# Kernel tuning notes

Measured on AMD Instinct MI355X. Metric: run time of the kernel, lower is better.

Reference implementation:

```python
import jax, jax.numpy as jnp
import numpy as np

B, N, D = 4, 4096, 512          # batch, seq_len, hidden_size
H, DH = 8, 64                    # n_heads, head_dim
M = 512                          # nb_features = 0.125 * seq_len
LN_EPS = 1e-12
KERNEL_EPS = 1e-4


def setup_inputs() -> dict:
    key = jax.random.key(0)
    ks = jax.random.split(key, 12)
    s = 0.02
    return {
        "input_tensor": jax.random.normal(ks[0], (B, N, D), jnp.float32),
        "attention_mask": jnp.zeros((B, 1, 1, N), jnp.float32),  # unused by module
        "Wq": jax.random.normal(ks[1], (D, D), jnp.float32) * s,
        "bq": jnp.zeros((D,), jnp.float32),
        "Wk": jax.random.normal(ks[2], (D, D), jnp.float32) * s,
        "bk": jnp.zeros((D,), jnp.float32),
        "Wv": jax.random.normal(ks[3], (D, D), jnp.float32) * s,
        "bv": jnp.zeros((D,), jnp.float32),
        # gaussian (orthogonal-style) random feature projections [M, DH]
        "proj_q": jax.random.normal(ks[4], (M, DH), jnp.float32),
        "proj_k": jax.random.normal(ks[5], (M, DH), jnp.float32),
        "Wd": jax.random.normal(ks[6], (D, D), jnp.float32) * s,
        "bd": jnp.zeros((D,), jnp.float32),
        "gamma": jnp.ones((D,), jnp.float32),
        "beta": jnp.zeros((D,), jnp.float32),
    }


def _softmax_kernel(data, projection_matrix, is_query):
    # data: [B,H,N,DH], projection_matrix: [M,DH]
    data_normalizer = data.shape[-1] ** (-0.25)
    ratio = projection_matrix.shape[0] ** (-0.5)
    data_dash = jnp.einsum("bhnd,md->bhnm", data_normalizer * data, projection_matrix)
    diag_data = (jnp.sum(data * data, axis=-1) * 0.5 * data_normalizer ** 2)[..., None]
    if is_query:
        stab = jnp.max(data_dash, axis=-1, keepdims=True)
    else:
        stab = jnp.max(data_dash)  # global max, per original code
    return ratio * (jnp.exp(data_dash - diag_data - stab) + KERNEL_EPS)


def _linear_attention(q, k, v):
    # q,k: [B,H,N,M]; v: [B,H,N,DH]
    k_cumsum = jnp.sum(k, axis=-2)                               # [B,H,M]
    d_inv = 1.0 / jnp.einsum("bhnm,bhm->bhn", q, k_cumsum)       # [B,H,N]
    context = jnp.einsum("bhnm,bhne->bhme", k, v)                # [B,H,M,DH]
    return jnp.einsum("bhme,bhnm,bhn->bhne", context, q, d_inv)  # [B,H,N,DH]


def reference(input_tensor, attention_mask, Wq, bq, Wk, bk, Wv, bv,
              proj_q, proj_k, Wd, bd, gamma, beta):
    def heads(x):  # [B,N,D] -> [B,H,N,DH]
        return x.reshape(B, N, H, DH).transpose(0, 2, 1, 3)

    q = heads(input_tensor @ Wq.T + bq)
    k = heads(input_tensor @ Wk.T + bk)
    v = heads(input_tensor @ Wv.T + bv)

    q = _softmax_kernel(q, proj_q, is_query=True)
    k = _softmax_kernel(k, proj_k, is_query=False)

    ctx = _linear_attention(q, k, v)                  # [B,H,N,DH]
    ctx = ctx.transpose(0, 2, 1, 3).reshape(B, N, D)  # merge heads

    hidden = ctx @ Wd.T + bd                          # dropout is identity (eval)
    x = hidden + input_tensor
    mu = jnp.mean(x, axis=-1, keepdims=True)
    var = jnp.mean((x - mu) ** 2, axis=-1, keepdims=True)
    return (x - mu) / jnp.sqrt(var + LN_EPS) * gamma + beta
```

## Files before the change

kernel.cpp:

```cpp
#include <hip/hip_runtime.h>
#include <math.h>

typedef __bf16 bf16;
typedef __bf16 bf16x8 __attribute__((ext_vector_type(8)));
typedef __bf16 bf16x4 __attribute__((ext_vector_type(4)));
typedef float  f32x4  __attribute__((ext_vector_type(4)));

#define NSEQ 4096
#define DMODEL 512
#define DHEAD 64
#define MFEAT 512
#define BHEADS 32
#define ROWS_TOTAL 16384

#define NORMALIZER 0.35355339059327373f
#define DIAG_C 0.0625f
#define KEPS 1e-4f

__device__ __forceinline__ float warpReduceSum(float v) {
#pragma unroll
    for (int off = 32; off > 0; off >>= 1) v += __shfl_xor(v, off);
    return v;
}

__device__ __forceinline__ void atomicMaxF(float* addr, float val) {
    int* ai = (int*)addr;
    int cur = __float_as_int(*addr);
    while (__int_as_float(cur) < val) {
        int prev = atomicCAS(ai, cur, __float_as_int(val));
        if (prev == cur) break;
        cur = prev;
    }
}

__device__ __forceinline__ void gload16(const void* g, void* l) {
    __builtin_amdgcn_global_load_lds((const __attribute__((address_space(1))) void*)g,
                                     (__attribute__((address_space(3))) void*)l, 16, 0, 0);
}

__global__ __launch_bounds__(256)
void prep_convert(const float* __restrict__ x, const float* __restrict__ Wq,
                  const float* __restrict__ Wk, const float* __restrict__ Wv,
                  const float* __restrict__ Wd, const float* __restrict__ pq,
                  const float* __restrict__ bq, const float* __restrict__ bk,
                  const float* __restrict__ bv,
                  bf16* __restrict__ xb, bf16* __restrict__ Wb,
                  bf16* __restrict__ Wdb, bf16* __restrict__ pqb,
                  float* __restrict__ bcat)
{
    size_t i4 = (size_t)blockIdx.x * 256 + threadIdx.x;
    size_t e0 = i4 * 4;
    if (e0 >= 9471488) return;
    const float* src;
    if (e0 < 8388608) {
        src = x + e0;
        float4 v = *(const float4*)src;
        bf16* d = xb + e0;
        d[0] = (bf16)v.x; d[1] = (bf16)v.y; d[2] = (bf16)v.z; d[3] = (bf16)v.w;
    } else if (e0 < 9175040) {
        size_t c = e0 - 8388608; int wsel = (int)(c >> 18); size_t o = c & 262143;
        src = (wsel == 0 ? Wq : wsel == 1 ? Wk : Wv) + o;
        float4 v = *(const float4*)src;
        bf16* d = Wb + c;
        d[0] = (bf16)v.x; d[1] = (bf16)v.y; d[2] = (bf16)v.z; d[3] = (bf16)v.w;
    } else if (e0 < 9437184) {
        size_t c = e0 - 9175040;
        src = Wd + c;
        float4 v = *(const float4*)src;
        bf16* d = Wdb + c;
        d[0] = (bf16)v.x; d[1] = (bf16)v.y; d[2] = (bf16)v.z; d[3] = (bf16)v.w;
    } else if (e0 < 9469952) {
        size_t c = e0 - 9437184;
        src = pq + c;
        float4 v = *(const float4*)src;
        const int feat = (int)(c >> 6), col = (int)(c & 63);
        bf16x4 d4;
        d4[0] = (bf16)v.x; d4[1] = (bf16)v.y; d4[2] = (bf16)v.z; d4[3] = (bf16)v.w;
        const int inrow = (col << 1) ^ ((feat & 7) << 4);
        *(bf16x4*)((char*)pqb + (size_t)feat * 128 + inrow) = d4;
    } else {
        size_t c = e0 - 9469952; int wsel = (int)(c >> 9); size_t o = c & 511;
        src = (wsel == 0 ? bq : wsel == 1 ? bk : bv) + o;
        *(float4*)(bcat + c) = *(const float4*)src;
    }
}

template<int MODE>
__global__ __launch_bounds__(256)
void gemm_mfma(const bf16* __restrict__ A, const bf16* __restrict__ Bw,
               const float* __restrict__ bias, const float* __restrict__ resid,
               bf16* __restrict__ outQ, bf16* __restrict__ outK,
               bf16* __restrict__ outV, float* __restrict__ outF)
{
    __shared__ char As[16384];
    __shared__ char Bs[16384];
    const int tid = threadIdx.x;
    const int w = tid >> 6, l = tid & 63;
    const int wr = w >> 1, wc = w & 1;
    const int row0 = blockIdx.y << 7;
    const int col0 = blockIdx.x << 7;

    f32x4 acc[4][4] = {};
    const char* Ab = (const char*)A + (size_t)row0 * 1024;
    const char* Bb = (const char*)Bw + (size_t)col0 * 1024;

    for (int kt = 0; kt < 8; ++kt) {
        const int k0b = kt << 7;
#pragma unroll
        for (int i = 0; i < 4; ++i) {
            int off = (i << 12) + (tid << 4);
            int g = off ^ ((off >> 3) & 0x70);
            int grow = g >> 7, gcol = g & 127;
            gload16(Ab + (size_t)grow * 1024 + k0b + gcol, As + (i << 12) + (w << 10));
            gload16(Bb + (size_t)grow * 1024 + k0b + gcol, Bs + (i << 12) + (w << 10));
        }
        __syncthreads();
#pragma unroll
        for (int ks = 0; ks < 2; ++ks) {
            bf16x8 af[4], bb[4];
#pragma unroll
            for (int mi = 0; mi < 4; ++mi) {
                int row = (wr << 6) + (mi << 4) + (l & 15);
                int addr = ((row << 7) + (ks << 6) + ((l >> 4) << 4)) ^ ((row & 7) << 4);
                af[mi] = *(const bf16x8*)(As + addr);
            }
#pragma unroll
            for (int nj = 0; nj < 4; ++nj) {
                int row = (wc << 6) + (nj << 4) + (l & 15);
                int addr = ((row << 7) + (ks << 6) + ((l >> 4) << 4)) ^ ((row & 7) << 4);
                bb[nj] = *(const bf16x8*)(Bs + addr);
            }
#pragma unroll
            for (int mi = 0; mi < 4; ++mi)
#pragma unroll
                for (int nj = 0; nj < 4; ++nj)
                    acc[mi][nj] = __builtin_amdgcn_mfma_f32_16x16x32_bf16(af[mi], bb[nj], acc[mi][nj], 0, 0, 0);
        }
        __syncthreads();
    }

    const int subrow = (l >> 4) << 2;
    const int subcol = l & 15;
#pragma unroll
    for (int mi = 0; mi < 4; ++mi) {
#pragma unroll
        for (int nj = 0; nj < 4; ++nj) {
            const int cg = col0 + (wc << 6) + (nj << 4) + subcol;
            const float bi = bias[cg];
            const int rgb = row0 + (wr << 6) + (mi << 4) + subrow;
            if (MODE == 0) {
                if (cg < 512) {
                    const int hh = cg >> 6, ee = cg & 63;
                    const int bb2 = rgb >> 12, n = rgb & 4095;
#pragma unroll
                    for (int r = 0; r < 4; ++r)
                        outQ[((size_t)((bb2 * 8 + hh) * 4096 + n + r)) * 64 + ee] =
                            (bf16)(acc[mi][nj][r] + bi);
                } else if (cg < 1024) {
                    const int eg = cg - 512, hh = eg >> 6, ee = eg & 63;
#pragma unroll
                    for (int r = 0; r < 4; ++r) {
                        const int rg = rgb + r;
                        *(bf16*)((char*)outK + (size_t)rg * 1024 + hh * 128 +
                                 ((ee * 2) ^ ((rg & 7) << 4))) = (bf16)(acc[mi][nj][r] + bi);
                    }
                } else {
                    const int eg = cg - 1024, hh = eg >> 6, ee = eg & 63;
                    const int bb2 = rgb >> 12, n = rgb & 4095;
                    bf16x4 pv;
#pragma unroll
                    for (int r = 0; r < 4; ++r) pv[r] = (bf16)(acc[mi][nj][r] + bi);
                    const int nb = n * 2;
                    size_t byteaddr = (size_t)((bb2 * 8 + hh) * 64 + ee) * 8192
                                    + (size_t)((nb & ~127) | ((nb & 127) ^ ((ee & 7) << 4)));
                    *(bf16x4*)((char*)outV + byteaddr) = pv;
                }
            } else {
#pragma unroll
                for (int r = 0; r < 4; ++r) {
                    const int rg = rgb + r;
                    outF[(size_t)rg * 512 + cg] = acc[mi][nj][r] + bi + resid[(size_t)rg * 512 + cg];
                }
            }
        }
    }
}

__global__ __launch_bounds__(64)
void vsum_kernel(const bf16* __restrict__ Vt, float* __restrict__ vsum)
{
    const int row = blockIdx.x;
    const bf16x8* p = (const bf16x8*)((const char*)Vt + (size_t)row * 8192);
    float s = 0.f;
#pragma unroll
    for (int i = 0; i < 8; ++i) {
        bf16x8 v = p[threadIdx.x + i * 64];
#pragma unroll
        for (int u = 0; u < 8; ++u) s += (float)v[u];
    }
    s = warpReduceSum(s);
    if (threadIdx.x == 0) vsum[row] = s;
}

__global__ __launch_bounds__(256)
void diag_kernel(const bf16* __restrict__ Kb, float* __restrict__ dgk)
{
    const int idx = blockIdx.x * 256 + threadIdx.x;
    const int bh = idx >> 12, n = idx & 4095;
    const int b = bh >> 3, h = bh & 7;
    const char* row = (const char*)Kb + (size_t)(b * 4096 + n) * 1024 + h * 128;
    const int sw = (n & 7) << 4;
    float ss = 0.f;
#pragma unroll
    for (int j = 0; j < 8; ++j) {
        bf16x8 v = *(const bf16x8*)(row + ((j << 4) ^ sw));
#pragma unroll
        for (int u = 0; u < 8; ++u) { float f = (float)v[u]; ss += f * f; }
    }
    dgk[idx] = DIAG_C * ss;
}

__global__ __launch_bounds__(512, 1)
void kside_mfma6(const bf16* __restrict__ Kb, const bf16* __restrict__ Vt,
                 const float* __restrict__ projk, const float* __restrict__ dgk,
                 float* __restrict__ ctxp4, float* __restrict__ esumf4,
                 float* __restrict__ gmax)
{
    __shared__ char K_s[16384];
    __shared__ char V_s[16384];
    __shared__ char E_s[32768];

    const int tid = threadIdx.x;
    const int w = tid >> 6, l = tid & 63;
    const int lq = l & 15, lg = l >> 4;
    const int bh = blockIdx.x;
    const int b = bh >> 3, h = bh & 7;
    const int mw = (blockIdx.y << 8) + (w << 5);
    const int z = blockIdx.z;
    const int swl = (lq & 7) << 4;

    bf16x8 pk[2][2];
#pragma unroll
    for (int mj = 0; mj < 2; ++mj)
#pragma unroll
        for (int ks = 0; ks < 2; ++ks) {
            const int m = mw + (mj << 4) + lq;
            const float* p = projk + (size_t)m * 64 + (ks << 5) + (lg << 3);
            float4 a = *(const float4*)p;
            float4 c = *(const float4*)(p + 4);
            bf16x8 f;
            f[0] = (bf16)a.x; f[1] = (bf16)a.y; f[2] = (bf16)a.z; f[3] = (bf16)a.w;
            f[4] = (bf16)c.x; f[5] = (bf16)c.y; f[6] = (bf16)c.z; f[7] = (bf16)c.w;
            pk[mj][ks] = f;
        }

    const char* kgb = (const char*)Kb + (size_t)(b * 4096) * 1024 + h * 128;
    const char* vgb = (const char*)Vt + (size_t)bh * 64 * 8192;
    const float* dgb = dgk + (bh << 12);
    const int trow = tid >> 3;
    const int tseg = (tid & 7) << 4;
    char* tw = E_s + (w << 12);

    f32x4 acc2[4][2] = {};
    float esacc[2] = {0.f, 0.f};
    float lmax = -1e30f;
    const f32x4 Zc = {0.f, 0.f, 0.f, 0.f};

    {
        const int nc = z << 10;
        gload16(kgb + (size_t)(nc + trow) * 1024 + tseg, K_s + (tid << 4));
        gload16(vgb + (size_t)trow * 8192 + (nc << 1) + tseg, V_s + (tid << 4));
    }

    int cur = 0;
    for (int c = 0; c < 16; ++c) {
        __syncthreads();
        if (c < 15) {
            const int nn = (z << 10) + ((c + 1) << 6);
            gload16(kgb + (size_t)(nn + trow) * 1024 + tseg,
                    K_s + ((cur ^ 1) << 13) + (tid << 4));
            gload16(vgb + (size_t)trow * 8192 + (nn << 1) + tseg,
                    V_s + ((cur ^ 1) << 13) + (tid << 4));
        }
        const char* Kc = K_s + (cur << 13);
        const char* Vc = V_s + (cur << 13);
        const int nc = (z << 10) + (c << 6);

        f32x4 acc1[4][2];
#pragma unroll
        for (int nt = 0; nt < 4; ++nt) {
            const char* kr = Kc + ((nt << 4) + lq) * 128;
            bf16x8 afk0 = *(const bf16x8*)(kr + ((lg << 4) ^ swl));
            bf16x8 afk1 = *(const bf16x8*)(kr + ((64 + (lg << 4)) ^ swl));
#pragma unroll
            for (int mj = 0; mj < 2; ++mj) {
                acc1[nt][mj] = __builtin_amdgcn_mfma_f32_16x16x32_bf16(afk0, pk[mj][0], Zc, 0, 0, 0);
                acc1[nt][mj] = __builtin_amdgcn_mfma_f32_16x16x32_bf16(afk1, pk[mj][1], acc1[nt][mj], 0, 0, 0);
            }
        }
#pragma unroll
        for (int nt = 0; nt < 4; ++nt) {
            float4 dv = *(const float4*)(dgb + nc + (nt << 4) + (lg << 2));
            const float dgr[4] = {dv.x, dv.y, dv.z, dv.w};
#pragma unroll
            for (int mj = 0; mj < 2; ++mj) {
                const int m = (mj << 4) + lq;
                bf16x4 ev;
#pragma unroll
                for (int r = 0; r < 4; ++r) {
                    float kd = NORMALIZER * acc1[nt][mj][r];
                    lmax = fmaxf(lmax, kd);
                    float e = __expf(kd - dgr[r]);
                    esacc[mj] += e;
                    ev[r] = (bf16)e;
                }
                *(bf16x4*)(tw + m * 128 + (((nt << 5) + (lg << 3)) ^ swl)) = ev;
            }
        }
#pragma unroll
        for (int ks2 = 0; ks2 < 2; ++ks2) {
            bf16x8 be[2];
#pragma unroll
            for (int mj = 0; mj < 2; ++mj) {
                const int m = (mj << 4) + lq;
                be[mj] = *(const bf16x8*)(tw + m * 128 + (((ks2 << 6) + (lg << 4)) ^ swl));
            }
#pragma unroll
            for (int et = 0; et < 4; ++et) {
                const int e = (et << 4) + lq;
                bf16x8 av = *(const bf16x8*)(Vc + e * 128 + (((ks2 << 6) + (lg << 4)) ^ swl));
#pragma unroll
                for (int mj = 0; mj < 2; ++mj)
                    acc2[et][mj] = __builtin_amdgcn_mfma_f32_16x16x32_bf16(av, be[mj], acc2[et][mj], 0, 0, 0);
            }
        }
        cur ^= 1;
    }

#pragma unroll
    for (int mj = 0; mj < 2; ++mj) {
        float s = esacc[mj];
        s += __shfl_xor(s, 16); s += __shfl_xor(s, 32);
        if (l < 16)
            esumf4[((size_t)z * 32 + bh) * 512 + mw + (mj << 4) + lq] = s;
    }
#pragma unroll
    for (int off = 32; off > 0; off >>= 1) lmax = fmaxf(lmax, __shfl_xor(lmax, off));
    if (l == 0) atomicMaxF(gmax, lmax);

    float* cz = ctxp4 + (size_t)z * (32 * 64 * 512) + (size_t)bh * 64 * 512;
#pragma unroll
    for (int et = 0; et < 4; ++et)
#pragma unroll
        for (int mj = 0; mj < 2; ++mj)
#pragma unroll
            for (int r = 0; r < 4; ++r) {
                const int e = (et << 4) + (lg << 2) + r;
                cz[(size_t)e * 512 + mw + (mj << 4) + lq] = acc2[et][mj][r];
            }
}

__global__ __launch_bounds__(256)
void finalize_ctx(const float* __restrict__ ctxp4, const float* __restrict__ esumf4,
                  bf16* __restrict__ ctxE, float* __restrict__ ctxsum,
                  float* __restrict__ esumsum)
{
    __shared__ float red_s[4][64];
    const int tid = threadIdx.x;
    const int bh = blockIdx.x;
    const int mc = blockIdx.y << 7;
    const int e = tid & 63, ms = tid >> 6;
    const size_t Z = (size_t)32 * 64 * 512;

    const float* cb = ctxp4 + (size_t)bh * 64 * 512 + (size_t)e * 512 + mc + (ms << 5);
    char* obr = (char*)ctxE + ((size_t)bh * 80 + e) * 1024;
    float s = 0.f;
#pragma unroll
    for (int i8 = 0; i8 < 4; ++i8) {
        float acc[8] = {};
#pragma unroll
        for (int zz = 0; zz < 4; ++zz) {
            float4 v0 = *(const float4*)(cb + zz * Z + (i8 << 3));
            float4 v1 = *(const float4*)(cb + zz * Z + (i8 << 3) + 4);
            acc[0] += v0.x; acc[1] += v0.y; acc[2] += v0.z; acc[3] += v0.w;
            acc[4] += v1.x; acc[5] += v1.y; acc[6] += v1.z; acc[7] += v1.w;
        }
        bf16x8 p8;
#pragma unroll
        for (int u = 0; u < 8; ++u) { s += acc[u]; p8[u] = (bf16)acc[u]; }
        const int mloc = mc + (ms << 5) + (i8 << 3);
        *(bf16x8*)(obr + ((mloc << 1) ^ ((e & 7) << 4))) = p8;
    }
    red_s[ms][e] = s;
    __syncthreads();
    if (tid < 64)
        atomicAdd(ctxsum + bh * 64 + tid,
                  red_s[0][tid] + red_s[1][tid] + red_s[2][tid] + red_s[3][tid]);
    if (tid < 128) {
        const int m = mc + tid;
        float ev = esumf4[(size_t)bh * 512 + m]
                 + esumf4[((size_t)32 + bh) * 512 + m]
                 + esumf4[((size_t)64 + bh) * 512 + m]
                 + esumf4[((size_t)96 + bh) * 512 + m];
        bf16* er = ctxE + (size_t)(bh * 80 + 64) * 512;
        er[m] = (bf16)1.0f;
        er[512 + (m ^ 8)] = (bf16)ev;
        float t = warpReduceSum(ev);
        if ((tid & 63) == 0) atomicAdd(esumsum + bh, t);
    }
}

__global__ __launch_bounds__(512, 1)
void qside_mfma4(const bf16* __restrict__ Qb, const bf16* __restrict__ Pq,
                 const bf16* __restrict__ CtxE, const float* __restrict__ vsum,
                 const float* __restrict__ ctxsum, const float* __restrict__ esumsum,
                 const float* __restrict__ gmax, bf16* __restrict__ OutC)
{
    __shared__ char ctx_s[81920];
    __shared__ char pq_s[2][16384];
    __shared__ char T_s[40960];

    const int tid = threadIdx.x;
    const int w = tid >> 6, l = tid & 63;
    const int lq = l & 15, lg = l >> 4;
    const int bh = blockIdx.x;
    const int b = bh >> 3, h = bh & 7;
    const int n0 = blockIdx.y << 9;

    const char* ctxg = (const char*)CtxE + (size_t)bh * 81920;
    const char* pqg  = (const char*)Pq;
#pragma unroll
    for (int i = 0; i < 10; ++i)
        gload16(ctxg + (i << 13) + (tid << 4), ctx_s + (i << 13) + (w << 10));
#pragma unroll
    for (int p = 0; p < 2; ++p)
        gload16(pqg + (p << 13) + (tid << 4), pq_s[0] + (p << 13) + (w << 10));

    const char* qgb = (const char*)Qb + ((size_t)bh * 4096 + n0 + (w << 6)) * 128;
    bf16x8 qa[4][2];
    float diag_l[4];
#pragma unroll
    for (int ni = 0; ni < 4; ++ni) {
        const char* qr = qgb + ((ni << 4) + lq) * 128;
        float ss = 0.f;
#pragma unroll
        for (int kk = 0; kk < 2; ++kk) {
            qa[ni][kk] = *(const bf16x8*)(qr + (kk << 6) + (lg << 4));
#pragma unroll
            for (int u = 0; u < 8; ++u) { float f = (float)qa[ni][kk][u]; ss += f * f; }
        }
        ss += __shfl_xor(ss, 16);
        ss += __shfl_xor(ss, 32);
        diag_l[ni] = DIAG_C * ss;
    }

    f32x4 acc2[4][5] = {};
    float mmax[4] = {-1e30f, -1e30f, -1e30f, -1e30f};
    char* tw = T_s + w * 5120;
    const f32x4 Zc = {0.f, 0.f, 0.f, 0.f};

    __syncthreads();

    for (int ft = 0; ft < 4; ++ft) {
        const int buf = ft & 1;
        if (ft < 3) {
#pragma unroll
            for (int p = 0; p < 2; ++p)
                gload16(pqg + ((ft + 1) << 14) + (p << 13) + (tid << 4),
                        pq_s[buf ^ 1] + (p << 13) + (w << 10));
        }
        const char* pqb = pq_s[buf];
#pragma unroll
        for (int sl = 0; sl < 4; ++sl) {
            f32x4 acc1[2][4];
#pragma unroll
            for (int mi = 0; mi < 2; ++mi) {
                const int fr = (sl << 5) + (mi << 4) + lq;
                bf16x8 pf = *(const bf16x8*)(pqb + fr * 128 +
                              (((lg << 4)) ^ ((lq & 7) << 4)));
#pragma unroll
                for (int ni = 0; ni < 4; ++ni)
                    acc1[mi][ni] = __builtin_amdgcn_mfma_f32_16x16x32_bf16(pf, qa[ni][0], Zc, 0, 0, 0);
            }
#pragma unroll
            for (int mi = 0; mi < 2; ++mi) {
                const int fr = (sl << 5) + (mi << 4) + lq;
                bf16x8 pf = *(const bf16x8*)(pqb + fr * 128 +
                              ((64 + (lg << 4)) ^ ((lq & 7) << 4)));
#pragma unroll
                for (int ni = 0; ni < 4; ++ni)
                    acc1[mi][ni] = __builtin_amdgcn_mfma_f32_16x16x32_bf16(pf, qa[ni][1], acc1[mi][ni], 0, 0, 0);
            }
#pragma unroll
            for (int mi = 0; mi < 2; ++mi)
#pragma unroll
                for (int ni = 0; ni < 4; ++ni) {
                    bf16x4 tv;
#pragma unroll
                    for (int r = 0; r < 4; ++r) {
                        const float qd = acc1[mi][ni][r];
                        mmax[ni] = fmaxf(mmax[ni], qd);
                        tv[r] = (bf16)__expf(NORMALIZER * qd - diag_l[ni]);
                    }
                    *(bf16x4*)(tw + ((ni << 4) + lq) * 80 + (mi << 5) + (lg << 3)) = tv;
                }
            bf16x8 ta[4];
#pragma unroll
            for (int ni = 0; ni < 4; ++ni)
                ta[ni] = *(const bf16x8*)(tw + ((ni << 4) + lq) * 80 + (lg << 4));
#pragma unroll
            for (int nj = 0; nj < 5; ++nj) {
                const int e = (nj << 4) + lq;
                bf16x8 cb = *(const bf16x8*)(ctx_s + e * 1024 +
                              (((ft << 8) + (sl << 6) + (lg << 4)) ^ ((e & 7) << 4)));
#pragma unroll
                for (int ni = 0; ni < 4; ++ni)
                    acc2[ni][nj] = __builtin_amdgcn_mfma_f32_16x16x32_bf16(ta[ni], cb, acc2[ni][nj], 0, 0, 0);
            }
        }
        __syncthreads();
    }

    const float sG = __expf(-gmax[0]);
    const float ess = esumsum[bh];
    bf16* outb = OutC + ((size_t)(b * 4096) + n0 + (w << 6)) * 512 + (h << 6);
#pragma unroll
    for (int ni = 0; ni < 4; ++ni) {
        float mmr = mmax[ni];
        mmr = fmaxf(mmr, __shfl_xor(mmr, 16));
        mmr = fmaxf(mmr, __shfl_xor(mmr, 32));
#pragma unroll
        for (int r = 0; r < 4; ++r) {
            const float mm = __shfl(mmr, (lg << 2) + r);
            const float uT = __shfl(acc2[ni][4][r], (lg << 4));
            const float uE = __shfl(acc2[ni][4][r], (lg << 4) | 1);
            const float cr = __expf(-NORMALIZER * mm);
            const float qsum = cr * uT + KEPS * 512.0f;
            const float D = sG * (cr * uE + KEPS * ess) + KEPS * 4096.0f * qsum;
            const float inv = 1.0f / D;
            const float al = sG * cr * inv;
            const float G1 = sG * KEPS * inv;
            const float G2 = KEPS * qsum * inv;
            const int row = (ni << 4) + (lg << 2) + r;
#pragma unroll
            for (int nj = 0; nj < 4; ++nj) {
                const int e = (nj << 4) + lq;
                float v = al * acc2[ni][nj][r] + G1 * ctxsum[(bh << 6) + e] + G2 * vsum[(bh << 6) + e];
                outb[(size_t)row * 512 + e] = (bf16)v;
            }
        }
    }
}

__global__ __launch_bounds__(256)
void ln_kernel(const float* __restrict__ hid, const float* __restrict__ gamma,
               const float* __restrict__ beta, float* __restrict__ out)
{
    const int row = (blockIdx.x << 2) + (threadIdx.x >> 6);
    const int lane = threadIdx.x & 63;
    const float* x = hid + (size_t)row * DMODEL + (lane << 3);
    float4 a = *(const float4*)x;
    float4 c = *(const float4*)(x + 4);
    float s = a.x + a.y + a.z + a.w + c.x + c.y + c.z + c.w;
    float sq = a.x * a.x + a.y * a.y + a.z * a.z + a.w * a.w +
               c.x * c.x + c.y * c.y + c.z * c.z + c.w * c.w;
    s = warpReduceSum(s);
    sq = warpReduceSum(sq);
    const float mu = s * 0.001953125f;
    const float var = sq * 0.001953125f - mu * mu;
    const float rs = rsqrtf(var + 1e-12f);
    const float4 g1 = *(const float4*)(gamma + (lane << 3));
    const float4 g2 = *(const float4*)(gamma + (lane << 3) + 4);
    const float4 b1 = *(const float4*)(beta + (lane << 3));
    const float4 b2 = *(const float4*)(beta + (lane << 3) + 4);
    float4 o1, o2;
    o1.x = (a.x - mu) * rs * g1.x + b1.x;
    o1.y = (a.y - mu) * rs * g1.y + b1.y;
    o1.z = (a.z - mu) * rs * g1.z + b1.z;
    o1.w = (a.w - mu) * rs * g1.w + b1.w;
    o2.x = (c.x - mu) * rs * g2.x + b2.x;
    o2.y = (c.y - mu) * rs * g2.y + b2.y;
    o2.z = (c.z - mu) * rs * g2.z + b2.z;
    o2.w = (c.w - mu) * rs * g2.w + b2.w;
    *(float4*)(out + (size_t)row * DMODEL + (lane << 3)) = o1;
    *(float4*)(out + (size_t)row * DMODEL + (lane << 3) + 4) = o2;
}

__global__ void init_misc(float* gmax)
{
    if (threadIdx.x == 0 && blockIdx.x == 0) *gmax = -1e30f;
}

extern "C" void kernel_launch(void* const* d_in, const int* in_sizes, int n_in,
                              void* d_out, int out_size, void* d_ws, size_t ws_size,
                              hipStream_t stream)
{
    const float* x     = (const float*)d_in[0];
    const float* Wq    = (const float*)d_in[2];
    const float* bq    = (const float*)d_in[3];
    const float* Wk    = (const float*)d_in[4];
    const float* bk    = (const float*)d_in[5];
    const float* Wv    = (const float*)d_in[6];
    const float* bv    = (const float*)d_in[7];
    const float* projq = (const float*)d_in[8];
    const float* projk = (const float*)d_in[9];
    const float* Wd    = (const float*)d_in[10];
    const float* bd    = (const float*)d_in[11];
    const float* gamma = (const float*)d_in[12];
    const float* beta  = (const float*)d_in[13];

    char* W = (char*)d_ws;
    bf16*  qb16   = (bf16*) (W);
    bf16*  kb16s  = (bf16*) (W + 16777216);
    bf16*  vtb    = (bf16*) (W + 33554432);
    bf16*  xb16   = (bf16*) (W + 50331648);
    float* hidf32 = (float*)(W + 67108864);
    float* ctxp4  = (float*)(W + 67108864);
    float* esumf4 = (float*)(W + 83886080);
    float* dgk    = (float*)(W + 84148224);
    bf16*  Wb16   = (bf16*) (W + 100663296);
    bf16*  Wdb16  = (bf16*) (W + 102236160);
    bf16*  pqb16  = (bf16*) (W + 102760448);
    float* bcat   = (float*)(W + 102825984);
    bf16*  ctxE   = (bf16*) (W + 102832128);
    float* vsumb  = (float*)(W + 105453568);
    float* ctxsum = (float*)(W + 105461760);
    float* esmsm  = (float*)(W + 105469952);
    float* gmaxb  = (float*)(W + 105470080);

    prep_convert<<<9250, 256, 0, stream>>>(x, Wq, Wk, Wv, Wd, projq, bq, bk, bv,
                                           xb16, Wb16, Wdb16, pqb16, bcat);
    hipMemsetAsync(ctxE, 0, 2621440, stream);
    hipMemsetAsync(ctxsum, 0, 8192 + 128, stream);
    init_misc<<<1, 64, 0, stream>>>(gmaxb);

    gemm_mfma<0><<<dim3(12, 128), 256, 0, stream>>>(xb16, Wb16, bcat, nullptr,
                                                    qb16, kb16s, vtb, nullptr);

    diag_kernel<<<512, 256, 0, stream>>>(kb16s, dgk);
    vsum_kernel<<<2048, 64, 0, stream>>>(vtb, vsumb);
    kside_mfma6<<<dim3(32, 2, 4), 512, 0, stream>>>(kb16s, vtb, projk, dgk,
                                                    ctxp4, esumf4, gmaxb);
    finalize_ctx<<<dim3(32, 4), 256, 0, stream>>>(ctxp4, esumf4, ctxE, ctxsum, esmsm);

    qside_mfma4<<<dim3(32, 8), 512, 0, stream>>>(qb16, pqb16, ctxE, vsumb,
                                                 ctxsum, esmsm, gmaxb, xb16);

    gemm_mfma<1><<<dim3(4, 128), 256, 0, stream>>>(xb16, Wdb16, bd, x,
                                                   nullptr, nullptr, nullptr, hidf32);
    ln_kernel<<<4096, 256, 0, stream>>>(hidf32, gamma, beta, (float*)d_out);
}
```

Before: 199.8 us.

## Widen per-warp feature tile in K-side kernel and split sequence eightfold

The K-side kernel now runs 256-thread blocks, two per CU. Each warp covers 64 random features instead of 32, so each K fragment read from LDS feeds twice as many MFMAs. The sequence is split into 8 chunks instead of 4, keeping the block count up, and finalize_ctx now sums 8 partial context and esum buffers. The data normalizer is folded into the bf16 projection weights, which removes a per-element multiply. In exchange, the partial-buffer traffic doubles, register pressure rises, and esum and dgk are placed over the already-consumed QKV weight buffer in the workspace.

```diff
diff --git a/kernel.cpp b/kernel.cpp
--- a/kernel.cpp
+++ b/kernel.cpp
@@ -220,10 +220,10 @@
     dgk[idx] = DIAG_C * ss;
 }
 
-__global__ __launch_bounds__(512, 1)
-void kside_mfma6(const bf16* __restrict__ Kb, const bf16* __restrict__ Vt,
+__global__ __launch_bounds__(256, 2)
+void kside_mfma7(const bf16* __restrict__ Kb, const bf16* __restrict__ Vt,
                  const float* __restrict__ projk, const float* __restrict__ dgk,
-                 float* __restrict__ ctxp4, float* __restrict__ esumf4,
+                 float* __restrict__ ctxp8, float* __restrict__ esumf8,
                  float* __restrict__ gmax)
 {
     __shared__ char K_s[16384];
@@ -235,13 +235,13 @@
     const int lq = l & 15, lg = l >> 4;
     const int bh = blockIdx.x;
     const int b = bh >> 3, h = bh & 7;
-    const int mw = (blockIdx.y << 8) + (w << 5);
+    const int mw = (blockIdx.y << 8) + (w << 6);
     const int z = blockIdx.z;
     const int swl = (lq & 7) << 4;
 
-    bf16x8 pk[2][2];
-#pragma unroll
-    for (int mj = 0; mj < 2; ++mj)
+    bf16x8 pk[4][2];
+#pragma unroll
+    for (int mj = 0; mj < 4; ++mj)
 #pragma unroll
         for (int ks = 0; ks < 2; ++ks) {
             const int m = mw + (mj << 4) + lq;
@@ -249,88 +249,94 @@
             float4 a = *(const float4*)p;
             float4 c = *(const float4*)(p + 4);
             bf16x8 f;
-            f[0] = (bf16)a.x; f[1] = (bf16)a.y; f[2] = (bf16)a.z; f[3] = (bf16)a.w;
-            f[4] = (bf16)c.x; f[5] = (bf16)c.y; f[6] = (bf16)c.z; f[7] = (bf16)c.w;
+            f[0] = (bf16)(NORMALIZER * a.x); f[1] = (bf16)(NORMALIZER * a.y);
+            f[2] = (bf16)(NORMALIZER * a.z); f[3] = (bf16)(NORMALIZER * a.w);
+            f[4] = (bf16)(NORMALIZER * c.x); f[5] = (bf16)(NORMALIZER * c.y);
+            f[6] = (bf16)(NORMALIZER * c.z); f[7] = (bf16)(NORMALIZER * c.w);
             pk[mj][ks] = f;
         }
 
     const char* kgb = (const char*)Kb + (size_t)(b * 4096) * 1024 + h * 128;
     const char* vgb = (const char*)Vt + (size_t)bh * 64 * 8192;
-    const float* dgb = dgk + (bh << 12);
-    const int trow = tid >> 3;
-    const int tseg = (tid & 7) << 4;
-    char* tw = E_s + (w << 12);
-
-    f32x4 acc2[4][2] = {};
-    float esacc[2] = {0.f, 0.f};
+    const float* dgb = dgk + (bh << 12) + (z << 9);
+    char* tw = E_s + (w << 13);
+    const f32x4 Zc = {0.f, 0.f, 0.f, 0.f};
+
+    f32x4 acc2[4][4] = {};
+    float esacc[4] = {0.f, 0.f, 0.f, 0.f};
     float lmax = -1e30f;
-    const f32x4 Zc = {0.f, 0.f, 0.f, 0.f};
 
     {
-        const int nc = z << 10;
-        gload16(kgb + (size_t)(nc + trow) * 1024 + tseg, K_s + (tid << 4));
-        gload16(vgb + (size_t)trow * 8192 + (nc << 1) + tseg, V_s + (tid << 4));
+        const int nc = z << 9;
+#pragma unroll
+        for (int i = 0; i < 2; ++i) {
+            const int lin = tid + (i << 8);
+            const int row = lin >> 3, seg = (lin & 7) << 4;
+            gload16(kgb + (size_t)(nc + row) * 1024 + seg, K_s + (lin << 4));
+            gload16(vgb + (size_t)row * 8192 + (nc << 1) + seg, V_s + (lin << 4));
+        }
     }
 
     int cur = 0;
-    for (int c = 0; c < 16; ++c) {
+    for (int c = 0; c < 8; ++c) {
         __syncthreads();
-        if (c < 15) {
-            const int nn = (z << 10) + ((c + 1) << 6);
-            gload16(kgb + (size_t)(nn + trow) * 1024 + tseg,
-                    K_s + ((cur ^ 1) << 13) + (tid << 4));
-            gload16(vgb + (size_t)trow * 8192 + (nn << 1) + tseg,
-                    V_s + ((cur ^ 1) << 13) + (tid << 4));
+        if (c < 7) {
+            const int nn = (z << 9) + ((c + 1) << 6);
+#pragma unroll
+            for (int i = 0; i < 2; ++i) {
+                const int lin = tid + (i << 8);
+                const int row = lin >> 3, seg = (lin & 7) << 4;
+                gload16(kgb + (size_t)(nn + row) * 1024 + seg,
+                        K_s + ((cur ^ 1) << 13) + (lin << 4));
+                gload16(vgb + (size_t)row * 8192 + (nn << 1) + seg,
+                        V_s + ((cur ^ 1) << 13) + (lin << 4));
+            }
         }
         const char* Kc = K_s + (cur << 13);
         const char* Vc = V_s + (cur << 13);
-        const int nc = (z << 10) + (c << 6);
-
-        f32x4 acc1[4][2];
+
 #pragma unroll
         for (int nt = 0; nt < 4; ++nt) {
-            const char* kr = Kc + ((nt << 4) + lq) * 128;
-            bf16x8 afk0 = *(const bf16x8*)(kr + ((lg << 4) ^ swl));
-            bf16x8 afk1 = *(const bf16x8*)(kr + ((64 + (lg << 4)) ^ swl));
-#pragma unroll
-            for (int mj = 0; mj < 2; ++mj) {
-                acc1[nt][mj] = __builtin_amdgcn_mfma_f32_16x16x32_bf16(afk0, pk[mj][0], Zc, 0, 0, 0);
-                acc1[nt][mj] = __builtin_amdgcn_mfma_f32_16x16x32_bf16(afk1, pk[mj][1], acc1[nt][mj], 0, 0, 0);
-            }
-        }
-#pragma unroll
-        for (int nt = 0; nt < 4; ++nt) {
-            float4 dv = *(const float4*)(dgb + nc + (nt << 4) + (lg << 2));
+            const char* kr = Kc + (((nt << 4) + lq) << 7);
+            bf16x8 a0 = *(const bf16x8*)(kr + ((lg << 4) ^ swl));
+            bf16x8 a1 = *(const bf16x8*)(kr + ((64 + (lg << 4)) ^ swl));
+            f32x4 acc1[4];
+#pragma unroll
+            for (int mj = 0; mj < 4; ++mj) {
+                acc1[mj] = __builtin_amdgcn_mfma_f32_16x16x32_bf16(a0, pk[mj][0], Zc, 0, 0, 0);
+                acc1[mj] = __builtin_amdgcn_mfma_f32_16x16x32_bf16(a1, pk[mj][1], acc1[mj], 0, 0, 0);
+            }
+            float4 dv = *(const float4*)(dgb + (c << 6) + (nt << 4) + (lg << 2));
             const float dgr[4] = {dv.x, dv.y, dv.z, dv.w};
 #pragma unroll
-            for (int mj = 0; mj < 2; ++mj) {
-                const int m = (mj << 4) + lq;
+            for (int mj = 0; mj < 4; ++mj) {
                 bf16x4 ev;
 #pragma unroll
                 for (int r = 0; r < 4; ++r) {
-                    float kd = NORMALIZER * acc1[nt][mj][r];
-                    lmax = fmaxf(lmax, kd);
-                    float e = __expf(kd - dgr[r]);
+                    const float d = acc1[mj][r];
+                    lmax = fmaxf(lmax, d);
+                    const float e = __expf(d - dgr[r]);
                     esacc[mj] += e;
                     ev[r] = (bf16)e;
                 }
-                *(bf16x4*)(tw + m * 128 + (((nt << 5) + (lg << 3)) ^ swl)) = ev;
+                *(bf16x4*)(tw + (((mj << 4) + lq) << 7) +
+                           (((nt << 5) + (lg << 3)) ^ swl)) = ev;
             }
         }
 #pragma unroll
         for (int ks2 = 0; ks2 < 2; ++ks2) {
-            bf16x8 be[2];
-#pragma unroll
-            for (int mj = 0; mj < 2; ++mj) {
-                const int m = (mj << 4) + lq;
-                be[mj] = *(const bf16x8*)(tw + m * 128 + (((ks2 << 6) + (lg << 4)) ^ swl));
-            }
+            bf16x8 be[4];
+#pragma unroll
+            for (int mj = 0; mj < 4; ++mj)
+                be[mj] = *(const bf16x8*)(tw + (((mj << 4) + lq) << 7) +
+                                          (((ks2 << 6) + (lg << 4)) ^ swl));
 #pragma unroll
             for (int et = 0; et < 4; ++et) {
                 const int e = (et << 4) + lq;
-                bf16x8 av = *(const bf16x8*)(Vc + e * 128 + (((ks2 << 6) + (lg << 4)) ^ swl));
-#pragma unroll
-                for (int mj = 0; mj < 2; ++mj)
+                bf16x8 av = *(const bf16x8*)(Vc + (e << 7) +
+                                             (((ks2 << 6) + (lg << 4)) ^ swl));
+#pragma unroll
+                for (int mj = 0; mj < 4; ++mj)
                     acc2[et][mj] = __builtin_amdgcn_mfma_f32_16x16x32_bf16(av, be[mj], acc2[et][mj], 0, 0, 0);
             }
         }
@@ -338,21 +344,21 @@
     }
 
 #pragma unroll
-    for (int mj = 0; mj < 2; ++mj) {
+    for (int mj = 0; mj < 4; ++mj) {
         float s = esacc[mj];
         s += __shfl_xor(s, 16); s += __shfl_xor(s, 32);
         if (l < 16)
-            esumf4[((size_t)z * 32 + bh) * 512 + mw + (mj << 4) + lq] = s;
+            esumf8[((size_t)z * 32 + bh) * 512 + mw + (mj << 4) + lq] = s;
     }
 #pragma unroll
     for (int off = 32; off > 0; off >>= 1) lmax = fmaxf(lmax, __shfl_xor(lmax, off));
     if (l == 0) atomicMaxF(gmax, lmax);
 
-    float* cz = ctxp4 + (size_t)z * (32 * 64 * 512) + (size_t)bh * 64 * 512;
+    float* cz = ctxp8 + (size_t)z * (32 * 64 * 512) + (size_t)bh * 64 * 512;
 #pragma unroll
     for (int et = 0; et < 4; ++et)
 #pragma unroll
-        for (int mj = 0; mj < 2; ++mj)
+        for (int mj = 0; mj < 4; ++mj)
 #pragma unroll
             for (int r = 0; r < 4; ++r) {
                 const int e = (et << 4) + (lg << 2) + r;
@@ -361,7 +367,7 @@
 }
 
 __global__ __launch_bounds__(256)
-void finalize_ctx(const float* __restrict__ ctxp4, const float* __restrict__ esumf4,
+void finalize_ctx(const float* __restrict__ ctxp8, const float* __restrict__ esumf8,
                   bf16* __restrict__ ctxE, float* __restrict__ ctxsum,
                   float* __restrict__ esumsum)
 {
@@ -372,14 +378,14 @@
     const int e = tid & 63, ms = tid >> 6;
     const size_t Z = (size_t)32 * 64 * 512;
 
-    const float* cb = ctxp4 + (size_t)bh * 64 * 512 + (size_t)e * 512 + mc + (ms << 5);
+    const float* cb = ctxp8 + (size_t)bh * 64 * 512 + (size_t)e * 512 + mc + (ms << 5);
     char* obr = (char*)ctxE + ((size_t)bh * 80 + e) * 1024;
     float s = 0.f;
 #pragma unroll
     for (int i8 = 0; i8 < 4; ++i8) {
         float acc[8] = {};
 #pragma unroll
-        for (int zz = 0; zz < 4; ++zz) {
+        for (int zz = 0; zz < 8; ++zz) {
             float4 v0 = *(const float4*)(cb + zz * Z + (i8 << 3));
             float4 v1 = *(const float4*)(cb + zz * Z + (i8 << 3) + 4);
             acc[0] += v0.x; acc[1] += v0.y; acc[2] += v0.z; acc[3] += v0.w;
@@ -398,10 +404,10 @@
                   red_s[0][tid] + red_s[1][tid] + red_s[2][tid] + red_s[3][tid]);
     if (tid < 128) {
         const int m = mc + tid;
-        float ev = esumf4[(size_t)bh * 512 + m]
-                 + esumf4[((size_t)32 + bh) * 512 + m]
-                 + esumf4[((size_t)64 + bh) * 512 + m]
-                 + esumf4[((size_t)96 + bh) * 512 + m];
+        float ev = 0.f;
+#pragma unroll
+        for (int zz = 0; zz < 8; ++zz)
+            ev += esumf8[((size_t)zz * 32 + bh) * 512 + m];
         bf16* er = ctxE + (size_t)(bh * 80 + 64) * 512;
         er[m] = (bf16)1.0f;
         er[512 + (m ^ 8)] = (bf16)ev;
@@ -615,9 +621,9 @@
     bf16*  vtb    = (bf16*) (W + 33554432);
     bf16*  xb16   = (bf16*) (W + 50331648);
     float* hidf32 = (float*)(W + 67108864);
-    float* ctxp4  = (float*)(W + 67108864);
-    float* esumf4 = (float*)(W + 83886080);
-    float* dgk    = (float*)(W + 84148224);
+    float* ctxp8  = (float*)(W + 67108864);
+    float* esumf8 = (float*)(W + 100663296);
+    float* dgk    = (float*)(W + 101187584);
     bf16*  Wb16   = (bf16*) (W + 100663296);
     bf16*  Wdb16  = (bf16*) (W + 102236160);
     bf16*  pqb16  = (bf16*) (W + 102760448);
@@ -639,9 +645,9 @@
 
     diag_kernel<<<512, 256, 0, stream>>>(kb16s, dgk);
     vsum_kernel<<<2048, 64, 0, stream>>>(vtb, vsumb);
-    kside_mfma6<<<dim3(32, 2, 4), 512, 0, stream>>>(kb16s, vtb, projk, dgk,
-                                                    ctxp4, esumf4, gmaxb);
-    finalize_ctx<<<dim3(32, 4), 256, 0, stream>>>(ctxp4, esumf4, ctxE, ctxsum, esmsm);
+    kside_mfma7<<<dim3(32, 2, 8), 256, 0, stream>>>(kb16s, vtb, projk, dgk,
+                                                    ctxp8, esumf8, gmaxb);
+    finalize_ctx<<<dim3(32, 4), 256, 0, stream>>>(ctxp8, esumf8, ctxE, ctxsum, esmsm);
 
     qside_mfma4<<<dim3(32, 8), 512, 0, stream>>>(qb16, pqb16, ctxE, vsumb,
                                                  ctxsum, esmsm, gmaxb, xb16);
```

Result: no change. 201.8 us (+1.0%).
